# Kernel tuning notes

Hardware: AMD Instinct MI355X
Metric: run time of the kernel (lower is better)

The kernel has to match this reference:

```python
import jax, jax.numpy as jnp
import numpy as np


def setup_inputs() -> dict:
    key = jax.random.key(0)
    x = jax.random.normal(key, (2, 8192, 64), dtype=jnp.float32)  # [B, T, D]
    return {"x": x}


def reference(x) -> jnp.ndarray:
    # scores[b, i, j] = <x[b,i], x[b,j]>  -> [B, T, T]
    scores = jnp.einsum('bid,bjd->bij', x, x)
    # softmax over dim=1 (the non-last axis), matching nn.Softmax(dim=1)
    y = jax.nn.softmax(scores, axis=1)
    # y @ x -> [B, T, D], then permute(0, 2, 1) -> [B, D, T]
    out = jnp.einsum('bij,bjd->bid', y, x)
    return jnp.transpose(out, (0, 2, 1))
```

## Files before the change

### kernel.cpp

```cpp
#include <hip/hip_runtime.h>
#include <hip/hip_bf16.h>

#define TT 8192
#define DD 64
#define BB 2
#define NROWS (BB * TT)

typedef __attribute__((ext_vector_type(8))) short bf16x8;
typedef __attribute__((ext_vector_type(4))) short bf16x4;
typedef __attribute__((ext_vector_type(4))) float f32x4;

#define MFMA32 __builtin_amdgcn_mfma_f32_16x16x32_bf16

static __device__ inline f32x4 pv_mfma16(bf16x4 a, bf16x4 b, f32x4 c) {
#if __has_builtin(__builtin_amdgcn_mfma_f32_16x16x16bf16_1k)
  return __builtin_amdgcn_mfma_f32_16x16x16bf16_1k(a, b, c, 0, 0, 0);
#else
  asm volatile("v_mfma_f32_16x16x16_bf16 %0, %1, %2, %0" : "+v"(c) : "v"(a), "v"(b));
  return c;
#endif
}

typedef __attribute__((address_space(1))) const unsigned int gu32;
typedef __attribute__((address_space(3))) unsigned int lu32;

__device__ inline void gld_lds16(const unsigned short* g, unsigned short* l) {
  __builtin_amdgcn_global_load_lds((gu32*)g, (lu32*)l, 16, 0, 0);
}


__device__ inline unsigned short f2bf(float f) {
  unsigned int u = __float_as_uint(f);
  u += 0x7FFF + ((u >> 16) & 1);
  return (unsigned short)(u >> 16);
}
__device__ inline float bf2f(unsigned short h) {
  return __uint_as_float(((unsigned int)h) << 16);
}
__device__ inline unsigned int pk2bf(float lo, float hi) {
  __hip_bfloat162 h = __float22bfloat162_rn(float2{lo, hi});
  union { __hip_bfloat162 h; unsigned int u; } cv;
  cv.h = h;
  return cv.u;
}

__global__ __launch_bounds__(256) void ka_init(const float* __restrict__ x,
                                               unsigned short* __restrict__ xb,
                                               unsigned short* __restrict__ xt,
                                               float* __restrict__ m) {
  __shared__ __align__(16) unsigned short tile[64 * 72];
  int t = threadIdx.x;
  int r0 = blockIdx.x * 64;
  int rloc = t >> 2, part = t & 3;
  int r = r0 + rloc;
  const float4* px = (const float4*)(x + (size_t)r * DD + part * 16);
  unsigned short h[16];
  float msum = 0.f;
#pragma unroll
  for (int g = 0; g < 4; ++g) {
    float4 v = px[g];
    unsigned short h0 = f2bf(v.x), h1 = f2bf(v.y), h2 = f2bf(v.z), h3 = f2bf(v.w);
    h[g * 4 + 0] = h0; h[g * 4 + 1] = h1; h[g * 4 + 2] = h2; h[g * 4 + 3] = h3;
    float f0 = bf2f(h0), f1 = bf2f(h1), f2 = bf2f(h2), f3 = bf2f(h3);
    msum += f0 * f0 + f1 * f1 + f2 * f2 + f3 * f3;
  }
  uint4* xbr = (uint4*)(xb + (size_t)r * DD + part * 16);
#pragma unroll
  for (int g = 0; g < 2; ++g) {
    uint4 v;
    v.x = (unsigned int)h[g * 8 + 0] | ((unsigned int)h[g * 8 + 1] << 16);
    v.y = (unsigned int)h[g * 8 + 2] | ((unsigned int)h[g * 8 + 3] << 16);
    v.z = (unsigned int)h[g * 8 + 4] | ((unsigned int)h[g * 8 + 5] << 16);
    v.w = (unsigned int)h[g * 8 + 6] | ((unsigned int)h[g * 8 + 7] << 16);
    xbr[g] = v;
  }
#pragma unroll
  for (int k = 0; k < 16; ++k) tile[(part * 16 + k) * 72 + rloc] = h[k];
  msum += __shfl_xor(msum, 1, 64);
  msum += __shfl_xor(msum, 2, 64);
  if (part == 0) m[r] = msum;
  __syncthreads();
  int d = t >> 2, seg = t & 3;
  int b = r0 >> 13;
  int tcol = (r0 & (TT - 1)) + seg * 16;
  uint4 v0 = *(uint4*)(tile + d * 72 + seg * 16);
  uint4 v1 = *(uint4*)(tile + d * 72 + seg * 16 + 8);
  uint4* dst = (uint4*)(xt + ((size_t)b * DD + d) * TT + tcol);
  dst[0] = v0;
  dst[1] = v1;
}

__global__ __launch_bounds__(512, 2) void kb_l(const unsigned short* __restrict__ xq,
                                               const float* __restrict__ m,
                                               float* __restrict__ mm) {
  __shared__ __align__(16) unsigned short kslab[8][2][2048];
  __shared__ float lpart[8][32];
  int w = threadIdx.x >> 6, lane = threadIdx.x & 63;
  int c = lane & 15, q = lane >> 4;
  int lid = blockIdx.x;
  int b = (lid >> 2) & 1;
  int tile = (lid & 3) | ((lid >> 3) << 2);
  int j0g = b * TT + tile * 32;
  bf16x8 a0[2], a1[2];
  f32x4 mv[2];
#pragma unroll
  for (int u = 0; u < 2; ++u) {
    const unsigned short* pr = xq + (size_t)(j0g + u * 16 + c) * DD + q * 8;
    a0[u] = *(const bf16x8*)pr;
    a1[u] = *(const bf16x8*)(pr + 32);
    mv[u] = *(const f32x4*)(m + j0g + u * 16 + 4 * q);
  }
  const unsigned short* xqb = xq + (size_t)(b * TT) * DD;
  int k0 = w * 1024;
  int srow = lane >> 3;
  int sch = (lane & 7) ^ srow;
  unsigned short* sb = &kslab[w][0][0];
  auto stage = [&](int buf, int kbase) {
#pragma unroll
    for (int t = 0; t < 4; ++t)
      gld_lds16(xqb + (size_t)(kbase + t * 8 + srow) * DD + sch * 8,
                sb + buf * 2048 + t * 512);
  };
  stage(0, k0);
  float ls[2][4] = {{0.f, 0.f, 0.f, 0.f}, {0.f, 0.f, 0.f, 0.f}};
  int o1 = (q ^ (c & 7)) * 8, o2 = ((q | 4) ^ (c & 7)) * 8;
  for (int it = 0; it < 32; ++it) {
    if (it < 31) {
      stage((it & 1) ^ 1, k0 + (it + 1) * 32);
      asm volatile("s_waitcnt vmcnt(4)" ::: "memory");
    } else {
      asm volatile("s_waitcnt vmcnt(0)" ::: "memory");
    }
    __builtin_amdgcn_sched_barrier(0);
    const unsigned short* kp = sb + (it & 1) * 2048;
    bf16x8 b00 = *(const bf16x8*)(kp + c * 64 + o1);
    bf16x8 b01 = *(const bf16x8*)(kp + c * 64 + o2);
    bf16x8 b10 = *(const bf16x8*)(kp + (c + 16) * 64 + o1);
    bf16x8 b11 = *(const bf16x8*)(kp + (c + 16) * 64 + o2);
    __builtin_amdgcn_s_setprio(1);
#pragma unroll
    for (int u = 0; u < 2; ++u) {
      f32x4 z = {0.f, 0.f, 0.f, 0.f};
      f32x4 acc0 = MFMA32(a0[u], b00, z, 0, 0, 0);
      acc0 = MFMA32(a1[u], b01, acc0, 0, 0, 0);
      f32x4 acc1 = MFMA32(a0[u], b10, z, 0, 0, 0);
      acc1 = MFMA32(a1[u], b11, acc1, 0, 0, 0);
#pragma unroll
      for (int e = 0; e < 4; ++e)
        ls[u][e] += __expf(acc0[e] - mv[u][e]) + __expf(acc1[e] - mv[u][e]);
    }
    __builtin_amdgcn_s_setprio(0);
  }
#pragma unroll
  for (int u = 0; u < 2; ++u)
#pragma unroll
    for (int e = 0; e < 4; ++e) {
      float v = ls[u][e];
      v += __shfl_xor(v, 1, 64);
      v += __shfl_xor(v, 2, 64);
      v += __shfl_xor(v, 4, 64);
      v += __shfl_xor(v, 8, 64);
      if (c == 0) lpart[w][u * 16 + 4 * q + e] = v;
    }
  __syncthreads();
  int t = threadIdx.x;
  if (t < 32) {
    float s = 0.f;
#pragma unroll
    for (int w2 = 0; w2 < 8; ++w2) s += lpart[w2][t];
    mm[j0g + t] = m[j0g + t] + __logf(s);
  }
}

__global__ __launch_bounds__(512, 2) void kc_out(const unsigned short* __restrict__ xq,
                                                 const unsigned short* __restrict__ xt,
                                                 const float* __restrict__ mm,
                                                 float* __restrict__ out) {
  __shared__ __align__(16) unsigned short smem[36864];
  int w = threadIdx.x >> 6, lane = threadIdx.x & 63;
  int c = lane & 15, q = lane >> 4;
  int lid = blockIdx.x;
  int b = (lid >> 2) & 1;
  int tile = (lid & 3) | ((lid >> 3) << 2);
  int i0 = tile * 32;
  bf16x8 bq0[2], bq1[2];
#pragma unroll
  for (int u = 0; u < 2; ++u) {
    const unsigned short* pr = xq + (size_t)(b * TT + i0 + u * 16 + c) * DD + q * 8;
    bq0[u] = *(const bf16x8*)pr;
    bq1[u] = *(const bf16x8*)(pr + 32);
  }
  f32x4 o[2][4];
#pragma unroll
  for (int u = 0; u < 2; ++u)
#pragma unroll
    for (int nt = 0; nt < 4; ++nt) o[u][nt] = (f32x4){0.f, 0.f, 0.f, 0.f};

  const unsigned short* xqb = xq + (size_t)(b * TT) * DD;
  const unsigned short* xtb = xt + (size_t)b * DD * TT;
  const float* mmb = mm + b * TT;
  int jq0 = w * 1024;
  unsigned short* asb = smem + w * 2048;
  unsigned short* vsb = smem + 16384 + w * 2048;
  int srow = lane >> 3;
  int sch = (lane & 7) ^ srow;
  int vrow = lane >> 1;
  int vg = (lane & 1) ^ (vrow & 1);
  auto stage = [&](int buf, int j) {
#pragma unroll
    for (int t = 0; t < 2; ++t)
      gld_lds16(xqb + (size_t)(j + t * 8 + srow) * DD + sch * 8,
                asb + buf * 1024 + t * 512);
#pragma unroll
    for (int t = 0; t < 2; ++t)
      gld_lds16(xtb + (size_t)(t * 32 + vrow) * TT + j + vg * 8,
                vsb + buf * 1024 + t * 512);
  };
  stage(0, jq0);
  f32x4 cmm = *(const f32x4*)(mmb + jq0 + 4 * q);

  int o1 = (q ^ (c & 7)) * 8, o2 = ((q | 4) ^ (c & 7)) * 8;
  int vglo = (((q >> 1) ^ (c & 1)) * 8) + (q & 1) * 4;

  for (int it = 0; it < 64; ++it) {
    int jc = jq0 + it * 16;
    f32x4 nmm = cmm;
    if (it < 63) {
      nmm = *(const f32x4*)(mmb + jc + 16 + 4 * q);
      stage((it & 1) ^ 1, jc + 16);
      asm volatile("s_waitcnt vmcnt(4)" ::: "memory");
    } else {
      asm volatile("s_waitcnt vmcnt(0)" ::: "memory");
    }
    __builtin_amdgcn_sched_barrier(0);
    const unsigned short* ap = asb + (it & 1) * 1024;
    const unsigned short* vp = vsb + (it & 1) * 1024;
    bf16x8 a00 = *(const bf16x8*)(ap + c * 64 + o1);
    bf16x8 a01 = *(const bf16x8*)(ap + c * 64 + o2);
    bf16x4 bv[4];
#pragma unroll
    for (int nt = 0; nt < 4; ++nt)
      bv[nt] = *(const bf16x4*)(vp + (nt * 16 + c) * 16 + vglo);
    __builtin_amdgcn_s_setprio(1);
#pragma unroll
    for (int u = 0; u < 2; ++u) {
      f32x4 z = {0.f, 0.f, 0.f, 0.f};
      f32x4 s0 = MFMA32(a00, bq0[u], z, 0, 0, 0);
      s0 = MFMA32(a01, bq1[u], s0, 0, 0, 0);
      float w00 = __expf(s0[0] - cmm[0]);
      float w01 = __expf(s0[1] - cmm[1]);
      float w02 = __expf(s0[2] - cmm[2]);
      float w03 = __expf(s0[3] - cmm[3]);
      union { unsigned int uu[2]; bf16x4 v; } plo;
      plo.uu[0] = pk2bf(w00, w01);
      plo.uu[1] = pk2bf(w02, w03);
#pragma unroll
      for (int nt = 0; nt < 4; ++nt)
        o[u][nt] = pv_mfma16(plo.v, bv[nt], o[u][nt]);
    }
    __builtin_amdgcn_s_setprio(0);
    cmm = nmm;
  }
  __syncthreads();
  float* ow = (float*)smem + w * 2304;
#pragma unroll
  for (int u = 0; u < 2; ++u)
#pragma unroll
    for (int nt = 0; nt < 4; ++nt)
      *(f32x4*)(ow + (nt * 16 + c) * 36 + u * 16 + 4 * q) = o[u][nt];
  __syncthreads();
  int t = threadIdx.x, d = t & 63, g = t >> 6;
  const float* sbase = (const float*)smem;
  f32x4 sA = {0.f, 0.f, 0.f, 0.f};
#pragma unroll
  for (int w2 = 0; w2 < 8; ++w2)
    sA += *(const f32x4*)(sbase + w2 * 2304 + d * 36 + g * 4);
  *(f32x4*)(out + ((size_t)(b * DD + d)) * TT + i0 + g * 4) = sA;
}

extern "C" void kernel_launch(void* const* d_in, const int* in_sizes, int n_in,
                              void* d_out, int out_size, void* d_ws, size_t ws_size,
                              hipStream_t stream) {
  const float* x = (const float*)d_in[0];
  float* out = (float*)d_out;
  unsigned short* xb = (unsigned short*)d_ws;
  unsigned short* xt = xb + (size_t)NROWS * DD;
  float* m = (float*)(xt + (size_t)NROWS * DD);
  float* mmv = m + NROWS;

  ka_init<<<NROWS / 64, 256, 0, stream>>>(x, xb, xt, m);
  kb_l<<<512, 512, 0, stream>>>(xb, m, mmv);
  kc_out<<<512, 512, 0, stream>>>(xb, xt, mmv, out);
}
```

Measured before the change: 175.3 us.

## Share K/V tiles across warps in block-wide LDS and split j range with atomics

Both the column-LSE kernel and the output kernel now stage a shared block-wide LDS tile that all 8 warps read, instead of each warp streaming its own private slab. Each block covers more rows (64 or 128), which cuts redundant global/L2 traffic per row. In the output kernel the j range is split across two blocks, and partial results are combined with float atomicAdd into an output buffer that kb_l zero-fills. The trade-offs are a block-wide __syncthreads with vmcnt(0) every iteration, half as many blocks (256), non-deterministic atomic accumulation, and extra atomic traffic.

```diff
diff --git a/kernel.cpp b/kernel.cpp
--- a/kernel.cpp
+++ b/kernel.cpp
@@ -92,47 +92,47 @@
 
 __global__ __launch_bounds__(512, 2) void kb_l(const unsigned short* __restrict__ xq,
                                                const float* __restrict__ m,
-                                               float* __restrict__ mm) {
-  __shared__ __align__(16) unsigned short kslab[8][2][2048];
+                                               float* __restrict__ mm,
+                                               float* __restrict__ outz) {
+  __shared__ __align__(16) unsigned short kslab[2][128 * 64];
   __shared__ float lpart[8][32];
+  {
+    size_t zb = ((size_t)blockIdx.x * 512 + threadIdx.x) * 8;
+    *(f32x4*)(outz + zb) = (f32x4){0.f, 0.f, 0.f, 0.f};
+    *(f32x4*)(outz + zb + 4) = (f32x4){0.f, 0.f, 0.f, 0.f};
+  }
   int w = threadIdx.x >> 6, lane = threadIdx.x & 63;
   int c = lane & 15, q = lane >> 4;
   int lid = blockIdx.x;
-  int b = (lid >> 2) & 1;
-  int tile = (lid & 3) | ((lid >> 3) << 2);
-  int j0g = b * TT + tile * 32;
+  int bb = lid >> 7;
+  int j0g = lid * 64;
+  int wj2 = w >> 2, wk = w & 3;
   bf16x8 a0[2], a1[2];
   f32x4 mv[2];
 #pragma unroll
   for (int u = 0; u < 2; ++u) {
-    const unsigned short* pr = xq + (size_t)(j0g + u * 16 + c) * DD + q * 8;
+    const unsigned short* pr = xq + (size_t)(j0g + wj2 * 32 + u * 16 + c) * DD + q * 8;
     a0[u] = *(const bf16x8*)pr;
     a1[u] = *(const bf16x8*)(pr + 32);
-    mv[u] = *(const f32x4*)(m + j0g + u * 16 + 4 * q);
-  }
-  const unsigned short* xqb = xq + (size_t)(b * TT) * DD;
-  int k0 = w * 1024;
+    mv[u] = *(const f32x4*)(m + j0g + wj2 * 32 + u * 16 + 4 * q);
+  }
+  const unsigned short* xqb = xq + (size_t)(bb * TT) * DD;
   int srow = lane >> 3;
   int sch = (lane & 7) ^ srow;
-  unsigned short* sb = &kslab[w][0][0];
-  auto stage = [&](int buf, int kbase) {
-#pragma unroll
-    for (int t = 0; t < 4; ++t)
-      gld_lds16(xqb + (size_t)(kbase + t * 8 + srow) * DD + sch * 8,
-                sb + buf * 2048 + t * 512);
+  auto stage = [&](int buf, int kc) {
+#pragma unroll
+    for (int t = 0; t < 2; ++t)
+      gld_lds16(xqb + (size_t)(kc + w * 16 + t * 8 + srow) * DD + sch * 8,
+                &kslab[buf][0] + w * 1024 + t * 512);
   };
-  stage(0, k0);
+  stage(0, 0);
+  asm volatile("s_waitcnt vmcnt(0)" ::: "memory");
+  __syncthreads();
   float ls[2][4] = {{0.f, 0.f, 0.f, 0.f}, {0.f, 0.f, 0.f, 0.f}};
   int o1 = (q ^ (c & 7)) * 8, o2 = ((q | 4) ^ (c & 7)) * 8;
-  for (int it = 0; it < 32; ++it) {
-    if (it < 31) {
-      stage((it & 1) ^ 1, k0 + (it + 1) * 32);
-      asm volatile("s_waitcnt vmcnt(4)" ::: "memory");
-    } else {
-      asm volatile("s_waitcnt vmcnt(0)" ::: "memory");
-    }
-    __builtin_amdgcn_sched_barrier(0);
-    const unsigned short* kp = sb + (it & 1) * 2048;
+  for (int ks = 0; ks < 64; ++ks) {
+    if (ks < 63) stage((ks & 1) ^ 1, (ks + 1) * 128);
+    const unsigned short* kp = &kslab[ks & 1][0] + wk * 2048;
     bf16x8 b00 = *(const bf16x8*)(kp + c * 64 + o1);
     bf16x8 b01 = *(const bf16x8*)(kp + c * 64 + o2);
     bf16x8 b10 = *(const bf16x8*)(kp + (c + 16) * 64 + o1);
@@ -150,6 +150,8 @@
         ls[u][e] += __expf(acc0[e] - mv[u][e]) + __expf(acc1[e] - mv[u][e]);
     }
     __builtin_amdgcn_s_setprio(0);
+    asm volatile("s_waitcnt vmcnt(0)" ::: "memory");
+    __syncthreads();
   }
 #pragma unroll
   for (int u = 0; u < 2; ++u)
@@ -164,10 +166,11 @@
     }
   __syncthreads();
   int t = threadIdx.x;
-  if (t < 32) {
+  if (t < 64) {
+    int jg = t >> 5;
     float s = 0.f;
 #pragma unroll
-    for (int w2 = 0; w2 < 8; ++w2) s += lpart[w2][t];
+    for (int k3 = 0; k3 < 4; ++k3) s += lpart[jg * 4 + k3][t & 31];
     mm[j0g + t] = m[j0g + t] + __logf(s);
   }
 }
@@ -180,13 +183,14 @@
   int w = threadIdx.x >> 6, lane = threadIdx.x & 63;
   int c = lane & 15, q = lane >> 4;
   int lid = blockIdx.x;
-  int b = (lid >> 2) & 1;
-  int tile = (lid & 3) | ((lid >> 3) << 2);
-  int i0 = tile * 32;
+  int it = lid >> 1, jh = lid & 1;
+  int bb = it >> 6;
+  int i0 = (it & 63) * 128;
+  int wi = w >> 1, wj = w & 1;
   bf16x8 bq0[2], bq1[2];
 #pragma unroll
   for (int u = 0; u < 2; ++u) {
-    const unsigned short* pr = xq + (size_t)(b * TT + i0 + u * 16 + c) * DD + q * 8;
+    const unsigned short* pr = xq + (size_t)(bb * TT + i0 + wi * 32 + u * 16 + c) * DD + q * 8;
     bq0[u] = *(const bf16x8*)pr;
     bq1[u] = *(const bf16x8*)(pr + 32);
   }
@@ -196,72 +200,82 @@
 #pragma unroll
     for (int nt = 0; nt < 4; ++nt) o[u][nt] = (f32x4){0.f, 0.f, 0.f, 0.f};
 
-  const unsigned short* xqb = xq + (size_t)(b * TT) * DD;
-  const unsigned short* xtb = xt + (size_t)b * DD * TT;
-  const float* mmb = mm + b * TT;
-  int jq0 = w * 1024;
-  unsigned short* asb = smem + w * 2048;
-  unsigned short* vsb = smem + 16384 + w * 2048;
+  const unsigned short* xqb = xq + (size_t)(bb * TT) * DD;
+  const unsigned short* xtb = xt + (size_t)bb * DD * TT;
+  const float* mmb = mm + bb * TT;
+  int j0 = jh * 4096;
+  unsigned short* asl = smem;
+  unsigned short* vsl = smem + 8192;
   int srow = lane >> 3;
   int sch = (lane & 7) ^ srow;
-  int vrow = lane >> 1;
-  int vg = (lane & 1) ^ (vrow & 1);
-  auto stage = [&](int buf, int j) {
-#pragma unroll
-    for (int t = 0; t < 2; ++t)
-      gld_lds16(xqb + (size_t)(j + t * 8 + srow) * DD + sch * 8,
-                asb + buf * 1024 + t * 512);
-#pragma unroll
-    for (int t = 0; t < 2; ++t)
-      gld_lds16(xtb + (size_t)(t * 32 + vrow) * TT + j + vg * 8,
-                vsb + buf * 1024 + t * 512);
+  auto stage = [&](int buf, int jc) {
+    gld_lds16(xqb + (size_t)(jc + w * 8 + srow) * DD + sch * 8,
+              asl + buf * 4096 + w * 512);
+    gld_lds16(xtb + (size_t)(w * 8 + srow) * TT + jc + sch * 8,
+              vsl + buf * 4096 + w * 512);
   };
-  stage(0, jq0);
-  f32x4 cmm = *(const f32x4*)(mmb + jq0 + 4 * q);
-
+  stage(0, j0);
+  f32x4 cmm0 = *(const f32x4*)(mmb + j0 + wj * 32 + 4 * q);
+  f32x4 cmm1 = *(const f32x4*)(mmb + j0 + wj * 32 + 16 + 4 * q);
+  asm volatile("s_waitcnt vmcnt(0)" ::: "memory");
+  __syncthreads();
   int o1 = (q ^ (c & 7)) * 8, o2 = ((q | 4) ^ (c & 7)) * 8;
-  int vglo = (((q >> 1) ^ (c & 1)) * 8) + (q & 1) * 4;
-
-  for (int it = 0; it < 64; ++it) {
-    int jc = jq0 + it * 16;
-    f32x4 nmm = cmm;
-    if (it < 63) {
-      nmm = *(const f32x4*)(mmb + jc + 16 + 4 * q);
-      stage((it & 1) ^ 1, jc + 16);
-      asm volatile("s_waitcnt vmcnt(4)" ::: "memory");
-    } else {
-      asm volatile("s_waitcnt vmcnt(0)" ::: "memory");
+
+  for (int js = 0; js < 64; ++js) {
+    int jc = j0 + js * 64;
+    f32x4 nmm0 = cmm0, nmm1 = cmm1;
+    if (js < 63) {
+      stage((js & 1) ^ 1, jc + 64);
+      nmm0 = *(const f32x4*)(mmb + jc + 64 + wj * 32 + 4 * q);
+      nmm1 = *(const f32x4*)(mmb + jc + 64 + wj * 32 + 16 + 4 * q);
     }
-    __builtin_amdgcn_sched_barrier(0);
-    const unsigned short* ap = asb + (it & 1) * 1024;
-    const unsigned short* vp = vsb + (it & 1) * 1024;
+    const unsigned short* ap = asl + (js & 1) * 4096 + wj * 2048;
+    const unsigned short* vp = vsl + (js & 1) * 4096;
     bf16x8 a00 = *(const bf16x8*)(ap + c * 64 + o1);
     bf16x8 a01 = *(const bf16x8*)(ap + c * 64 + o2);
-    bf16x4 bv[4];
-#pragma unroll
-    for (int nt = 0; nt < 4; ++nt)
-      bv[nt] = *(const bf16x4*)(vp + (nt * 16 + c) * 16 + vglo);
+    bf16x8 a10 = *(const bf16x8*)(ap + (c + 16) * 64 + o1);
+    bf16x8 a11 = *(const bf16x8*)(ap + (c + 16) * 64 + o2);
+    bf16x4 bv[2][4];
+#pragma unroll
+    for (int jj = 0; jj < 2; ++jj)
+#pragma unroll
+      for (int nt = 0; nt < 4; ++nt) {
+        int pg = (wj * 4 + jj * 2 + (q >> 1)) ^ (c & 7);
+        bv[jj][nt] = *(const bf16x4*)(vp + (nt * 16 + c) * 64 + pg * 8 + (q & 1) * 4);
+      }
     __builtin_amdgcn_s_setprio(1);
 #pragma unroll
     for (int u = 0; u < 2; ++u) {
       f32x4 z = {0.f, 0.f, 0.f, 0.f};
       f32x4 s0 = MFMA32(a00, bq0[u], z, 0, 0, 0);
       s0 = MFMA32(a01, bq1[u], s0, 0, 0, 0);
-      float w00 = __expf(s0[0] - cmm[0]);
-      float w01 = __expf(s0[1] - cmm[1]);
-      float w02 = __expf(s0[2] - cmm[2]);
-      float w03 = __expf(s0[3] - cmm[3]);
-      union { unsigned int uu[2]; bf16x4 v; } plo;
-      plo.uu[0] = pk2bf(w00, w01);
-      plo.uu[1] = pk2bf(w02, w03);
-#pragma unroll
-      for (int nt = 0; nt < 4; ++nt)
-        o[u][nt] = pv_mfma16(plo.v, bv[nt], o[u][nt]);
+      f32x4 s1 = MFMA32(a10, bq0[u], z, 0, 0, 0);
+      s1 = MFMA32(a11, bq1[u], s1, 0, 0, 0);
+      float w00 = __expf(s0[0] - cmm0[0]);
+      float w01 = __expf(s0[1] - cmm0[1]);
+      float w02 = __expf(s0[2] - cmm0[2]);
+      float w03 = __expf(s0[3] - cmm0[3]);
+      float w10 = __expf(s1[0] - cmm1[0]);
+      float w11 = __expf(s1[1] - cmm1[1]);
+      float w12 = __expf(s1[2] - cmm1[2]);
+      float w13 = __expf(s1[3] - cmm1[3]);
+      union { unsigned int uu[2]; bf16x4 v; } pA, pB;
+      pA.uu[0] = pk2bf(w00, w01);
+      pA.uu[1] = pk2bf(w02, w03);
+      pB.uu[0] = pk2bf(w10, w11);
+      pB.uu[1] = pk2bf(w12, w13);
+#pragma unroll
+      for (int nt = 0; nt < 4; ++nt) {
+        o[u][nt] = pv_mfma16(pA.v, bv[0][nt], o[u][nt]);
+        o[u][nt] = pv_mfma16(pB.v, bv[1][nt], o[u][nt]);
+      }
     }
     __builtin_amdgcn_s_setprio(0);
-    cmm = nmm;
-  }
-  __syncthreads();
+    cmm0 = nmm0;
+    cmm1 = nmm1;
+    asm volatile("s_waitcnt vmcnt(0)" ::: "memory");
+    __syncthreads();
+  }
   float* ow = (float*)smem + w * 2304;
 #pragma unroll
   for (int u = 0; u < 2; ++u)
@@ -271,11 +285,16 @@
   __syncthreads();
   int t = threadIdx.x, d = t & 63, g = t >> 6;
   const float* sbase = (const float*)smem;
-  f32x4 sA = {0.f, 0.f, 0.f, 0.f};
-#pragma unroll
-  for (int w2 = 0; w2 < 8; ++w2)
-    sA += *(const f32x4*)(sbase + w2 * 2304 + d * 36 + g * 4);
-  *(f32x4*)(out + ((size_t)(b * DD + d)) * TT + i0 + g * 4) = sA;
+#pragma unroll
+  for (int wi2 = 0; wi2 < 4; ++wi2) {
+    f32x4 sA = *(const f32x4*)(sbase + (wi2 * 2 + 0) * 2304 + d * 36 + g * 4);
+    sA += *(const f32x4*)(sbase + (wi2 * 2 + 1) * 2304 + d * 36 + g * 4);
+    size_t ob = ((size_t)(bb * DD + d)) * TT + i0 + wi2 * 32 + g * 4;
+    atomicAdd(out + ob + 0, sA[0]);
+    atomicAdd(out + ob + 1, sA[1]);
+    atomicAdd(out + ob + 2, sA[2]);
+    atomicAdd(out + ob + 3, sA[3]);
+  }
 }
 
 extern "C" void kernel_launch(void* const* d_in, const int* in_sizes, int n_in,
@@ -289,6 +308,6 @@
   float* mmv = m + NROWS;
 
   ka_init<<<NROWS / 64, 256, 0, stream>>>(x, xb, xt, m);
-  kb_l<<<512, 512, 0, stream>>>(xb, m, mmv);
-  kc_out<<<512, 512, 0, stream>>>(xb, xt, mmv, out);
-}
+  kb_l<<<256, 512, 0, stream>>>(xb, m, mmv, out);
+  kc_out<<<256, 512, 0, stream>>>(xb, xt, mmv, out);
+}
```

Result: slower. 268.0 us (+52.9%).

## Retile logsumexp kernel to 64 columns per block and restage PV loads

Applied to the files above, without the earlier changes.

kb_l now handles 64 query columns per 1024-thread block with 16 waves, so each staged K tile is reused across four 16-row fragments instead of two. kc_out stages only the A operand through LDS, 32 rows per step. The V operand and the column stats are loaded straight into registers with inline global_load_dwordx2/x4 in a manually double-buffered, ping-pong pipeline. The aim is to cut LDS traffic and loop overhead and to keep more loads in flight. The cost is higher register pressure and lower occupancy.

```diff
diff --git a/kernel.cpp b/kernel.cpp
--- a/kernel.cpp
+++ b/kernel.cpp
@@ -90,28 +90,28 @@
   dst[1] = v1;
 }
 
-__global__ __launch_bounds__(512, 2) void kb_l(const unsigned short* __restrict__ xq,
-                                               const float* __restrict__ m,
-                                               float* __restrict__ mm) {
-  __shared__ __align__(16) unsigned short kslab[8][2][2048];
-  __shared__ float lpart[8][32];
+__global__ __launch_bounds__(1024, 1) void kb_l(const unsigned short* __restrict__ xq,
+                                                const float* __restrict__ m,
+                                                float* __restrict__ mm) {
+  __shared__ __align__(16) unsigned short kslab[16][2][2048];
+  __shared__ float lpart[16][64];
   int w = threadIdx.x >> 6, lane = threadIdx.x & 63;
   int c = lane & 15, q = lane >> 4;
   int lid = blockIdx.x;
-  int b = (lid >> 2) & 1;
-  int tile = (lid & 3) | ((lid >> 3) << 2);
-  int j0g = b * TT + tile * 32;
-  bf16x8 a0[2], a1[2];
-  f32x4 mv[2];
-#pragma unroll
-  for (int u = 0; u < 2; ++u) {
+  int b = lid >> 7;
+  int jt = lid & 127;
+  int j0g = b * TT + jt * 64;
+  bf16x8 a0[4], a1[4];
+  f32x4 mv[4];
+#pragma unroll
+  for (int u = 0; u < 4; ++u) {
     const unsigned short* pr = xq + (size_t)(j0g + u * 16 + c) * DD + q * 8;
     a0[u] = *(const bf16x8*)pr;
     a1[u] = *(const bf16x8*)(pr + 32);
     mv[u] = *(const f32x4*)(m + j0g + u * 16 + 4 * q);
   }
   const unsigned short* xqb = xq + (size_t)(b * TT) * DD;
-  int k0 = w * 1024;
+  int k0 = w * 512;
   int srow = lane >> 3;
   int sch = (lane & 7) ^ srow;
   unsigned short* sb = &kslab[w][0][0];
@@ -122,10 +122,14 @@
                 sb + buf * 2048 + t * 512);
   };
   stage(0, k0);
-  float ls[2][4] = {{0.f, 0.f, 0.f, 0.f}, {0.f, 0.f, 0.f, 0.f}};
+  float ls[4][4];
+#pragma unroll
+  for (int u = 0; u < 4; ++u)
+#pragma unroll
+    for (int e = 0; e < 4; ++e) ls[u][e] = 0.f;
   int o1 = (q ^ (c & 7)) * 8, o2 = ((q | 4) ^ (c & 7)) * 8;
-  for (int it = 0; it < 32; ++it) {
-    if (it < 31) {
+  for (int it = 0; it < 16; ++it) {
+    if (it < 15) {
       stage((it & 1) ^ 1, k0 + (it + 1) * 32);
       asm volatile("s_waitcnt vmcnt(4)" ::: "memory");
     } else {
@@ -139,7 +143,7 @@
     bf16x8 b11 = *(const bf16x8*)(kp + (c + 16) * 64 + o2);
     __builtin_amdgcn_s_setprio(1);
 #pragma unroll
-    for (int u = 0; u < 2; ++u) {
+    for (int u = 0; u < 4; ++u) {
       f32x4 z = {0.f, 0.f, 0.f, 0.f};
       f32x4 acc0 = MFMA32(a0[u], b00, z, 0, 0, 0);
       acc0 = MFMA32(a1[u], b01, acc0, 0, 0, 0);
@@ -152,7 +156,7 @@
     __builtin_amdgcn_s_setprio(0);
   }
 #pragma unroll
-  for (int u = 0; u < 2; ++u)
+  for (int u = 0; u < 4; ++u)
 #pragma unroll
     for (int e = 0; e < 4; ++e) {
       float v = ls[u][e];
@@ -164,18 +168,18 @@
     }
   __syncthreads();
   int t = threadIdx.x;
-  if (t < 32) {
+  if (t < 64) {
     float s = 0.f;
 #pragma unroll
-    for (int w2 = 0; w2 < 8; ++w2) s += lpart[w2][t];
+    for (int w2 = 0; w2 < 16; ++w2) s += lpart[w2][t];
     mm[j0g + t] = m[j0g + t] + __logf(s);
   }
 }
 
-__global__ __launch_bounds__(512, 2) void kc_out(const unsigned short* __restrict__ xq,
-                                                 const unsigned short* __restrict__ xt,
-                                                 const float* __restrict__ mm,
-                                                 float* __restrict__ out) {
+__global__ __launch_bounds__(512) void kc_out(const unsigned short* __restrict__ xq,
+                                              const unsigned short* __restrict__ xt,
+                                              const float* __restrict__ mm,
+                                              float* __restrict__ out) {
   __shared__ __align__(16) unsigned short smem[36864];
   int w = threadIdx.x >> 6, lane = threadIdx.x & 63;
   int c = lane & 15, q = lane >> 4;
@@ -200,67 +204,91 @@
   const unsigned short* xtb = xt + (size_t)b * DD * TT;
   const float* mmb = mm + b * TT;
   int jq0 = w * 1024;
-  unsigned short* asb = smem + w * 2048;
-  unsigned short* vsb = smem + 16384 + w * 2048;
+  unsigned short* asb = smem + w * 4096;
   int srow = lane >> 3;
   int sch = (lane & 7) ^ srow;
-  int vrow = lane >> 1;
-  int vg = (lane & 1) ^ (vrow & 1);
-  auto stage = [&](int buf, int j) {
-#pragma unroll
-    for (int t = 0; t < 2; ++t)
-      gld_lds16(xqb + (size_t)(j + t * 8 + srow) * DD + sch * 8,
-                asb + buf * 1024 + t * 512);
-#pragma unroll
-    for (int t = 0; t < 2; ++t)
-      gld_lds16(xtb + (size_t)(t * 32 + vrow) * TT + j + vg * 8,
-                vsb + buf * 1024 + t * 512);
-  };
-  stage(0, jq0);
-  f32x4 cmm = *(const f32x4*)(mmb + jq0 + 4 * q);
-
+  const unsigned short* pv0 = xtb + (size_t)c * TT + 4 * q;
   int o1 = (q ^ (c & 7)) * 8, o2 = ((q | 4) ^ (c & 7)) * 8;
-  int vglo = (((q >> 1) ^ (c & 1)) * 8) + (q & 1) * 4;
-
-  for (int it = 0; it < 64; ++it) {
-    int jc = jq0 + it * 16;
-    f32x4 nmm = cmm;
-    if (it < 63) {
-      nmm = *(const f32x4*)(mmb + jc + 16 + 4 * q);
-      stage((it & 1) ^ 1, jc + 16);
-      asm volatile("s_waitcnt vmcnt(4)" ::: "memory");
-    } else {
-      asm volatile("s_waitcnt vmcnt(0)" ::: "memory");
-    }
-    __builtin_amdgcn_sched_barrier(0);
-    const unsigned short* ap = asb + (it & 1) * 1024;
-    const unsigned short* vp = vsb + (it & 1) * 1024;
-    bf16x8 a00 = *(const bf16x8*)(ap + c * 64 + o1);
-    bf16x8 a01 = *(const bf16x8*)(ap + c * 64 + o2);
-    bf16x4 bv[4];
-#pragma unroll
-    for (int nt = 0; nt < 4; ++nt)
-      bv[nt] = *(const bf16x4*)(vp + (nt * 16 + c) * 16 + vglo);
-    __builtin_amdgcn_s_setprio(1);
-#pragma unroll
-    for (int u = 0; u < 2; ++u) {
-      f32x4 z = {0.f, 0.f, 0.f, 0.f};
-      f32x4 s0 = MFMA32(a00, bq0[u], z, 0, 0, 0);
-      s0 = MFMA32(a01, bq1[u], s0, 0, 0, 0);
-      float w00 = __expf(s0[0] - cmm[0]);
-      float w01 = __expf(s0[1] - cmm[1]);
-      float w02 = __expf(s0[2] - cmm[2]);
-      float w03 = __expf(s0[3] - cmm[3]);
-      union { unsigned int uu[2]; bf16x4 v; } plo;
-      plo.uu[0] = pk2bf(w00, w01);
-      plo.uu[1] = pk2bf(w02, w03);
-#pragma unroll
-      for (int nt = 0; nt < 4; ++nt)
-        o[u][nt] = pv_mfma16(plo.v, bv[nt], o[u][nt]);
-    }
-    __builtin_amdgcn_s_setprio(0);
-    cmm = nmm;
-  }
+
+  unsigned long long vA0[2], vA1[2], vA2[2], vA3[2];
+  unsigned long long vB0[2], vB1[2], vB2[2], vB3[2];
+  f32x4 pm0[2], pm1[2];
+
+#define KC_ISSUE(S, jn) do { \
+    __builtin_amdgcn_sched_barrier(0); \
+    gld_lds16(xqb + (size_t)((jn) + 0 + srow) * DD + sch * 8, asb + (S) * 2048 + 0); \
+    gld_lds16(xqb + (size_t)((jn) + 8 + srow) * DD + sch * 8, asb + (S) * 2048 + 512); \
+    gld_lds16(xqb + (size_t)((jn) + 16 + srow) * DD + sch * 8, asb + (S) * 2048 + 1024); \
+    gld_lds16(xqb + (size_t)((jn) + 24 + srow) * DD + sch * 8, asb + (S) * 2048 + 1536); \
+    __builtin_amdgcn_sched_barrier(0); \
+    { const unsigned short* pj = pv0 + (jn); \
+      asm volatile("global_load_dwordx2 %0, %1, off" : "=v"(vA0[S]) : "v"(pj)); \
+      asm volatile("global_load_dwordx2 %0, %1, off" : "=v"(vA1[S]) : "v"(pj + 16 * TT)); \
+      asm volatile("global_load_dwordx2 %0, %1, off" : "=v"(vA2[S]) : "v"(pj + 32 * TT)); \
+      asm volatile("global_load_dwordx2 %0, %1, off" : "=v"(vA3[S]) : "v"(pj + 48 * TT)); \
+      asm volatile("global_load_dwordx2 %0, %1, off" : "=v"(vB0[S]) : "v"(pj + 16)); \
+      asm volatile("global_load_dwordx2 %0, %1, off" : "=v"(vB1[S]) : "v"(pj + 16 * TT + 16)); \
+      asm volatile("global_load_dwordx2 %0, %1, off" : "=v"(vB2[S]) : "v"(pj + 32 * TT + 16)); \
+      asm volatile("global_load_dwordx2 %0, %1, off" : "=v"(vB3[S]) : "v"(pj + 48 * TT + 16)); \
+      asm volatile("global_load_dwordx4 %0, %1, off" : "=v"(pm0[S]) : "v"(mmb + (jn) + 4 * q)); \
+      asm volatile("global_load_dwordx4 %0, %1, off" : "=v"(pm1[S]) : "v"(mmb + (jn) + 16 + 4 * q)); } \
+    __builtin_amdgcn_sched_barrier(0); \
+  } while (0)
+#define KC_WAIT(N) do { \
+    asm volatile("s_waitcnt vmcnt(" #N ")" ::: "memory"); \
+    __builtin_amdgcn_sched_barrier(0); \
+  } while (0)
+#define KC_BODY(S) do { \
+    const unsigned short* ap = asb + (S) * 2048; \
+    bf16x8 a00 = *(const bf16x8*)(ap + c * 64 + o1); \
+    bf16x8 a01 = *(const bf16x8*)(ap + c * 64 + o2); \
+    bf16x8 a10 = *(const bf16x8*)(ap + (c + 16) * 64 + o1); \
+    bf16x8 a11 = *(const bf16x8*)(ap + (c + 16) * 64 + o2); \
+    union { unsigned long long u; bf16x4 v; } l0_, l1_, l2_, l3_, h0_, h1_, h2_, h3_; \
+    l0_.u = vA0[S]; l1_.u = vA1[S]; l2_.u = vA2[S]; l3_.u = vA3[S]; \
+    h0_.u = vB0[S]; h1_.u = vB1[S]; h2_.u = vB2[S]; h3_.u = vB3[S]; \
+    f32x4 cmm0 = pm0[S], cmm1 = pm1[S]; \
+    __builtin_amdgcn_s_setprio(1); \
+    _Pragma("unroll") for (int u = 0; u < 2; ++u) { \
+      f32x4 z = {0.f, 0.f, 0.f, 0.f}; \
+      f32x4 s0 = MFMA32(a00, bq0[u], z, 0, 0, 0); \
+      s0 = MFMA32(a01, bq1[u], s0, 0, 0, 0); \
+      f32x4 s1 = MFMA32(a10, bq0[u], z, 0, 0, 0); \
+      s1 = MFMA32(a11, bq1[u], s1, 0, 0, 0); \
+      float w00 = __expf(s0[0] - cmm0[0]); \
+      float w01 = __expf(s0[1] - cmm0[1]); \
+      float w02 = __expf(s0[2] - cmm0[2]); \
+      float w03 = __expf(s0[3] - cmm0[3]); \
+      float w10 = __expf(s1[0] - cmm1[0]); \
+      float w11 = __expf(s1[1] - cmm1[1]); \
+      float w12 = __expf(s1[2] - cmm1[2]); \
+      float w13 = __expf(s1[3] - cmm1[3]); \
+      union { unsigned int uu[2]; bf16x4 v; } pA, pB; \
+      pA.uu[0] = pk2bf(w00, w01); \
+      pA.uu[1] = pk2bf(w02, w03); \
+      pB.uu[0] = pk2bf(w10, w11); \
+      pB.uu[1] = pk2bf(w12, w13); \
+      o[u][0] = pv_mfma16(pA.v, l0_.v, o[u][0]); \
+      o[u][1] = pv_mfma16(pA.v, l1_.v, o[u][1]); \
+      o[u][2] = pv_mfma16(pA.v, l2_.v, o[u][2]); \
+      o[u][3] = pv_mfma16(pA.v, l3_.v, o[u][3]); \
+      o[u][0] = pv_mfma16(pB.v, h0_.v, o[u][0]); \
+      o[u][1] = pv_mfma16(pB.v, h1_.v, o[u][1]); \
+      o[u][2] = pv_mfma16(pB.v, h2_.v, o[u][2]); \
+      o[u][3] = pv_mfma16(pB.v, h3_.v, o[u][3]); \
+    } \
+    __builtin_amdgcn_s_setprio(0); \
+  } while (0)
+
+  KC_ISSUE(0, jq0);
+  for (int g = 0; g < 15; ++g) {
+    int jb = jq0 + g * 64;
+    KC_ISSUE(1, jb + 32); KC_WAIT(14); KC_BODY(0);
+    KC_ISSUE(0, jb + 64); KC_WAIT(14); KC_BODY(1);
+  }
+  KC_ISSUE(1, jq0 + 992); KC_WAIT(14); KC_BODY(0);
+  KC_WAIT(0); KC_BODY(1);
+
   __syncthreads();
   float* ow = (float*)smem + w * 2304;
 #pragma unroll
@@ -289,6 +317,6 @@
   float* mmv = m + NROWS;
 
   ka_init<<<NROWS / 64, 256, 0, stream>>>(x, xb, xt, m);
-  kb_l<<<512, 512, 0, stream>>>(xb, m, mmv);
+  kb_l<<<256, 1024, 0, stream>>>(xb, m, mmv);
   kc_out<<<512, 512, 0, stream>>>(xb, xt, mmv, out);
 }
```

Result: slower. 228.7 us (+30.4%).

## Stage V tile via register loads and padded LDS writes in kc_out

Applied to the files above, without the earlier changes.

The xt (V) tile is no longer staged with direct global-to-LDS loads. Each lane now loads its own row through global_load_dwordx4 into registers and writes it to a padded LDS layout (stride 24), which avoids the XOR swizzle. The mm values are fetched in the same batch, and the loop is unrolled by two with explicit vmcnt waits to pipeline loads against compute. The cost is more LDS and more registers, plus fragile hand-counted waitcnt ordering.

```diff
diff --git a/kernel.cpp b/kernel.cpp
--- a/kernel.cpp
+++ b/kernel.cpp
@@ -176,7 +176,7 @@
                                                  const unsigned short* __restrict__ xt,
                                                  const float* __restrict__ mm,
                                                  float* __restrict__ out) {
-  __shared__ __align__(16) unsigned short smem[36864];
+  __shared__ __align__(16) unsigned short smem[40960];
   int w = threadIdx.x >> 6, lane = threadIdx.x & 63;
   int c = lane & 15, q = lane >> 4;
   int lid = blockIdx.x;
@@ -201,66 +201,87 @@
   const float* mmb = mm + b * TT;
   int jq0 = w * 1024;
   unsigned short* asb = smem + w * 2048;
-  unsigned short* vsb = smem + 16384 + w * 2048;
+  unsigned short* vsb = smem + 16384 + w * 3072;
   int srow = lane >> 3;
   int sch = (lane & 7) ^ srow;
-  int vrow = lane >> 1;
-  int vg = (lane & 1) ^ (vrow & 1);
-  auto stage = [&](int buf, int j) {
-#pragma unroll
-    for (int t = 0; t < 2; ++t)
-      gld_lds16(xqb + (size_t)(j + t * 8 + srow) * DD + sch * 8,
-                asb + buf * 1024 + t * 512);
-#pragma unroll
-    for (int t = 0; t < 2; ++t)
-      gld_lds16(xtb + (size_t)(t * 32 + vrow) * TT + j + vg * 8,
-                vsb + buf * 1024 + t * 512);
-  };
-  stage(0, jq0);
-  f32x4 cmm = *(const f32x4*)(mmb + jq0 + 4 * q);
-
+  const unsigned short* pvrow = xtb + (size_t)lane * TT;
   int o1 = (q ^ (c & 7)) * 8, o2 = ((q | 4) ^ (c & 7)) * 8;
-  int vglo = (((q >> 1) ^ (c & 1)) * 8) + (q & 1) * 4;
-
-  for (int it = 0; it < 64; ++it) {
-    int jc = jq0 + it * 16;
-    f32x4 nmm = cmm;
-    if (it < 63) {
-      nmm = *(const f32x4*)(mmb + jc + 16 + 4 * q);
-      stage((it & 1) ^ 1, jc + 16);
-      asm volatile("s_waitcnt vmcnt(4)" ::: "memory");
-    } else {
-      asm volatile("s_waitcnt vmcnt(0)" ::: "memory");
-    }
-    __builtin_amdgcn_sched_barrier(0);
-    const unsigned short* ap = asb + (it & 1) * 1024;
-    const unsigned short* vp = vsb + (it & 1) * 1024;
-    bf16x8 a00 = *(const bf16x8*)(ap + c * 64 + o1);
-    bf16x8 a01 = *(const bf16x8*)(ap + c * 64 + o2);
-    bf16x4 bv[4];
-#pragma unroll
-    for (int nt = 0; nt < 4; ++nt)
-      bv[nt] = *(const bf16x4*)(vp + (nt * 16 + c) * 16 + vglo);
-    __builtin_amdgcn_s_setprio(1);
-#pragma unroll
-    for (int u = 0; u < 2; ++u) {
-      f32x4 z = {0.f, 0.f, 0.f, 0.f};
-      f32x4 s0 = MFMA32(a00, bq0[u], z, 0, 0, 0);
-      s0 = MFMA32(a01, bq1[u], s0, 0, 0, 0);
-      float w00 = __expf(s0[0] - cmm[0]);
-      float w01 = __expf(s0[1] - cmm[1]);
-      float w02 = __expf(s0[2] - cmm[2]);
-      float w03 = __expf(s0[3] - cmm[3]);
-      union { unsigned int uu[2]; bf16x4 v; } plo;
-      plo.uu[0] = pk2bf(w00, w01);
-      plo.uu[1] = pk2bf(w02, w03);
-#pragma unroll
-      for (int nt = 0; nt < 4; ++nt)
-        o[u][nt] = pv_mfma16(plo.v, bv[nt], o[u][nt]);
-    }
-    __builtin_amdgcn_s_setprio(0);
-    cmm = nmm;
-  }
+
+  f32x4 vA0, vB0, pmS0, vA1, vB1, pmS1;
+
+#define KC_ISSUE(VA, VB, PM, ABUF, jn) do { \
+    __builtin_amdgcn_sched_barrier(0); \
+    { const unsigned short* pj = pvrow + (jn); \
+      asm volatile("global_load_dwordx4 %0, %1, off" : "=v"(VA) : "v"(pj)); \
+      asm volatile("global_load_dwordx4 %0, %1, off" : "=v"(VB) : "v"(pj + 8)); \
+      asm volatile("global_load_dwordx4 %0, %1, off" : "=v"(PM) : "v"(mmb + (jn) + 4 * q)); } \
+    __builtin_amdgcn_sched_barrier(0); \
+    gld_lds16(xqb + (size_t)((jn) + srow) * DD + sch * 8, asb + (ABUF) * 1024); \
+    gld_lds16(xqb + (size_t)((jn) + 8 + srow) * DD + sch * 8, asb + (ABUF) * 1024 + 512); \
+    __builtin_amdgcn_sched_barrier(0); \
+  } while (0)
+#define KC_WAIT(N) do { \
+    asm volatile("s_waitcnt vmcnt(" #N ")" ::: "memory"); \
+    __builtin_amdgcn_sched_barrier(0); \
+  } while (0)
+#define KC_VWRITE(VA, VB, VBUF) do { \
+    unsigned short* vw = vsb + (VBUF) * 1536 + lane * 24; \
+    *(f32x4*)vw = VA; \
+    *(f32x4*)(vw + 8) = VB; \
+  } while (0)
+#define KC_BODY(ABUF, VBUF, PM) do { \
+    const unsigned short* ap = asb + (ABUF) * 1024; \
+    const unsigned short* vp = vsb + (VBUF) * 1536; \
+    bf16x8 a00 = *(const bf16x8*)(ap + c * 64 + o1); \
+    bf16x8 a01 = *(const bf16x8*)(ap + c * 64 + o2); \
+    bf16x4 bv[4]; \
+    _Pragma("unroll") for (int nt = 0; nt < 4; ++nt) \
+      bv[nt] = *(const bf16x4*)(vp + (nt * 16 + c) * 24 + 4 * q); \
+    f32x4 cmm = PM; \
+    __builtin_amdgcn_s_setprio(1); \
+    _Pragma("unroll") for (int u = 0; u < 2; ++u) { \
+      f32x4 z = {0.f, 0.f, 0.f, 0.f}; \
+      f32x4 s0 = MFMA32(a00, bq0[u], z, 0, 0, 0); \
+      s0 = MFMA32(a01, bq1[u], s0, 0, 0, 0); \
+      float w00 = __expf(s0[0] - cmm[0]); \
+      float w01 = __expf(s0[1] - cmm[1]); \
+      float w02 = __expf(s0[2] - cmm[2]); \
+      float w03 = __expf(s0[3] - cmm[3]); \
+      union { unsigned int uu[2]; bf16x4 v; } plo; \
+      plo.uu[0] = pk2bf(w00, w01); \
+      plo.uu[1] = pk2bf(w02, w03); \
+      o[u][0] = pv_mfma16(plo.v, bv[0], o[u][0]); \
+      o[u][1] = pv_mfma16(plo.v, bv[1], o[u][1]); \
+      o[u][2] = pv_mfma16(plo.v, bv[2], o[u][2]); \
+      o[u][3] = pv_mfma16(plo.v, bv[3], o[u][3]); \
+    } \
+    __builtin_amdgcn_s_setprio(0); \
+  } while (0)
+
+  KC_ISSUE(vA0, vB0, pmS0, 0, jq0);
+  KC_WAIT(3);
+  KC_VWRITE(vA0, vB0, 0);
+  for (int g = 0; g < 31; ++g) {
+    int jb = jq0 + g * 32;
+    KC_ISSUE(vA1, vB1, pmS1, 1, jb + 16);
+    KC_WAIT(5);
+    KC_BODY(0, 0, pmS0);
+    KC_WAIT(3);
+    KC_VWRITE(vA1, vB1, 1);
+    KC_ISSUE(vA0, vB0, pmS0, 0, jb + 32);
+    KC_WAIT(5);
+    KC_BODY(1, 1, pmS1);
+    KC_WAIT(3);
+    KC_VWRITE(vA0, vB0, 0);
+  }
+  KC_ISSUE(vA1, vB1, pmS1, 1, jq0 + 1008);
+  KC_WAIT(5);
+  KC_BODY(0, 0, pmS0);
+  KC_WAIT(3);
+  KC_VWRITE(vA1, vB1, 1);
+  KC_WAIT(0);
+  KC_BODY(1, 1, pmS1);
+
   __syncthreads();
   float* ow = (float*)smem + w * 2304;
 #pragma unroll
```

Measured after the change: 182.7 us. 4.2% more time.
